# Optimization experiments

Measured on AMD Instinct MI355X. Metric: run time of the kernel, lower is better.

## Reference

```python
import jax, jax.numpy as jnp
import numpy as np

N, D, H = 8192, 64, 256

def setup_inputs() -> dict:
    key = jax.random.key(0)
    k0, k1, k2, k3, k4 = jax.random.split(key, 5)
    y = jax.random.normal(k0, (N, D), jnp.float32)
    t = jax.random.uniform(k1, (1,), jnp.float32)
    # diffeq MLP params (time-conditioned 1-hidden-layer tanh net)
    W1 = jax.random.normal(k2, (D, H), jnp.float32) / np.float32(np.sqrt(D))
    b1 = jnp.zeros((H,), jnp.float32)
    wt = jax.random.normal(k3, (H,), jnp.float32) * jnp.float32(0.1)
    W2 = jax.random.normal(k4, (H, D), jnp.float32) / np.float32(np.sqrt(H))
    b2 = jnp.zeros((D,), jnp.float32)
    return {"t": t, "y": y, "W1": W1, "b1": b1, "wt": wt, "W2": W2, "b2": b2}

def reference(t, y, W1, b1, wt, W2, b2):
    ts = t[0]

    def f_single(yi):  # yi: [D] -> dy_i: [D]
        h = jnp.tanh(yi @ W1 + ts * wt + b1)
        return h @ W2 + b2

    # dy = diffeq(t, y): batched forward pass
    h = jnp.tanh(y @ W1 + ts * wt + b1)          # [N, H]
    dy = h @ W2 + b2                              # [N, D]

    # brute-force divergence = trace of per-sample Jacobian d(dy_i)/d(y_i)
    # (replaces the O(D) looped torch.autograd.grad calls with one batched
    #  forward-mode Jacobian computation)
    div = jax.vmap(lambda yi: jnp.trace(jax.jacfwd(f_single)(yi)))(y)  # [N]

    # original returns (dy, -divergence.view(N,1)); concatenated for a single output
    return jnp.concatenate([dy, -div[:, None]], axis=1)  # [N, D+1]
```

## Files before the change

### kernel.cpp

```cpp
#include <hip/hip_runtime.h>

#define NROWS 8192
#define DDIM 64
#define HDIM 256
#define W1S 260
#define W2S 68
#define HPAD 264

using bf16x8 = __attribute__((ext_vector_type(8))) short;
using f32x4  = __attribute__((ext_vector_type(4))) float;

__device__ __forceinline__ unsigned short f2bf(float x) {
    unsigned u = __float_as_uint(x);
    u += 0x7FFFu + ((u >> 16) & 1u);
    return (unsigned short)(u >> 16);
}
__device__ __forceinline__ unsigned pack2(float a, float b) {
    return (unsigned)f2bf(a) | ((unsigned)f2bf(b) << 16);
}
__device__ __forceinline__ float fast_tanh(float x) {
    float e = __expf(2.0f * x);
    return 1.0f - 2.0f * __builtin_amdgcn_rcpf(e + 1.0f);
}

__global__ __launch_bounds__(256)
void ode_fused(const float* __restrict__ t,
               const float* __restrict__ y,
               const float* __restrict__ W1,
               const float* __restrict__ b1,
               const float* __restrict__ wt,
               const float* __restrict__ W2,
               const float* __restrict__ b2,
               float* __restrict__ out) {
    const int tid  = threadIdx.x;
    const int w    = tid >> 6;
    const int lane = tid & 63;
    const int l16  = lane & 15;
    const int quad = lane >> 4;
    const int row0 = blockIdx.x * 16;

    __shared__ __align__(16) unsigned short w1s[64 * W1S];
    __shared__ __align__(16) unsigned short w2s[256 * W2S];
    __shared__ __align__(16) unsigned short h_lds[16 * HPAD];
    __shared__ float svs[HDIM];
    __shared__ float dvp[64];

    const float4* W1v = (const float4*)W1;
    const float4* W2v = (const float4*)W2;
    #pragma unroll
    for (int i = 0; i < 16; ++i) {
        float4 f = W1v[i * 256 + tid];
        int p = (i * 256 + tid) * 4;
        unsigned* dst = (unsigned*)&w1s[(p >> 8) * W1S + (p & 255)];
        dst[0] = pack2(f.x, f.y); dst[1] = pack2(f.z, f.w);
    }
    #pragma unroll
    for (int i = 0; i < 16; ++i) {
        float4 f = W2v[i * 256 + tid];
        int p = (i * 256 + tid) * 4;
        unsigned* dst = (unsigned*)&w2s[(p >> 6) * W2S + (p & 63)];
        dst[0] = pack2(f.x, f.y); dst[1] = pack2(f.z, f.w);
    }
    {
        float s = 0.f;
        #pragma unroll
        for (int k = 0; k < DDIM; ++k) s += W1[k * HDIM + tid] * W2[tid * DDIM + k];
        svs[tid] = s;
    }

    bf16x8 afr[2];
    const float* yrow = y + (size_t)(row0 + l16) * DDIM;
    #pragma unroll
    for (int ks = 0; ks < 2; ++ks) {
        float4 f0 = *(const float4*)(yrow + ks * 32 + quad * 8);
        float4 f1 = *(const float4*)(yrow + ks * 32 + quad * 8 + 4);
        bf16x8 a;
        a[0]=(short)f2bf(f0.x); a[1]=(short)f2bf(f0.y); a[2]=(short)f2bf(f0.z); a[3]=(short)f2bf(f0.w);
        a[4]=(short)f2bf(f1.x); a[5]=(short)f2bf(f1.y); a[6]=(short)f2bf(f1.z); a[7]=(short)f2bf(f1.w);
        afr[ks] = a;
    }

    const float ts = t[0];
    float cbv[4];
    #pragma unroll
    for (int ct = 0; ct < 4; ++ct) {
        int m = w * 64 + ct * 16 + l16;
        cbv[ct] = b1[m] + ts * wt[m];
    }
    const int ncol = w * 16 + l16;
    const float b2v = b2[ncol];

    __syncthreads();

    f32x4 acc[4];
    #pragma unroll
    for (int ct = 0; ct < 4; ++ct) acc[ct] = (f32x4){0.f, 0.f, 0.f, 0.f};
    #pragma unroll
    for (int ct = 0; ct < 4; ++ct) {
        const int m = w * 64 + ct * 16 + l16;
        #pragma unroll
        for (int ks = 0; ks < 2; ++ks) {
            bf16x8 b;
            #pragma unroll
            for (int j = 0; j < 8; ++j)
                b[j] = (short)w1s[(ks * 32 + quad * 8 + j) * W1S + m];
            acc[ct] = __builtin_amdgcn_mfma_f32_16x16x32_bf16(afr[ks], b, acc[ct], 0, 0, 0);
        }
    }

    float dv[4] = {0.f, 0.f, 0.f, 0.f};
    #pragma unroll
    for (int ct = 0; ct < 4; ++ct) {
        const int m = w * 64 + ct * 16 + l16;
        const float sv = svs[m];
        #pragma unroll
        for (int r = 0; r < 4; ++r) {
            float z = acc[ct][r] + cbv[ct];
            float h = fast_tanh(z);
            dv[r] += (1.f - h * h) * sv;
            h_lds[(quad * 4 + r) * HPAD + m] = f2bf(h);
        }
    }
    #pragma unroll
    for (int off = 8; off; off >>= 1) {
        #pragma unroll
        for (int r = 0; r < 4; ++r) dv[r] += __shfl_down(dv[r], off, 16);
    }
    if (l16 == 0) {
        #pragma unroll
        for (int r = 0; r < 4; ++r) dvp[w * 16 + quad * 4 + r] = dv[r];
    }
    __syncthreads();

    f32x4 acc2 = (f32x4){0.f, 0.f, 0.f, 0.f};
    #pragma unroll
    for (int ks = 0; ks < 8; ++ks) {
        bf16x8 a = *(const bf16x8*)(&h_lds[l16 * HPAD + ks * 32 + quad * 8]);
        bf16x8 b;
        #pragma unroll
        for (int j = 0; j < 8; ++j)
            b[j] = (short)w2s[(ks * 32 + quad * 8 + j) * W2S + ncol];
        acc2 = __builtin_amdgcn_mfma_f32_16x16x32_bf16(a, b, acc2, 0, 0, 0);
    }
    #pragma unroll
    for (int r = 0; r < 4; ++r) {
        const int row = quad * 4 + r;
        out[(size_t)(row0 + row) * (DDIM + 1) + ncol] = acc2[r] + b2v;
    }

    if (w == 0 && lane < 16) {
        float s = dvp[lane] + dvp[16 + lane] + dvp[32 + lane] + dvp[48 + lane];
        out[(size_t)(row0 + lane) * (DDIM + 1) + DDIM] = -s;
    }
}

extern "C" void kernel_launch(void* const* d_in, const int* in_sizes, int n_in,
                              void* d_out, int out_size, void* d_ws, size_t ws_size,
                              hipStream_t stream) {
    const float* t  = (const float*)d_in[0];
    const float* y  = (const float*)d_in[1];
    const float* W1 = (const float*)d_in[2];
    const float* b1 = (const float*)d_in[3];
    const float* wt = (const float*)d_in[4];
    const float* W2 = (const float*)d_in[5];
    const float* b2 = (const float*)d_in[6];
    float* out = (float*)d_out;

    ode_fused<<<NROWS / 16, 256, 0, stream>>>(t, y, W1, b1, wt, W2, b2, out);
}
```

Measured before the change: 75.76 us.

## Load weight fragments directly from global into registers, drop LDS weight staging

Each thread now loads only the W1 and W2 elements its MFMA B-fragments need straight from global memory into registers, removing the full-weight bf16 staging in LDS. LDS usage falls to the hidden-activation tile and a few small buffers, which should allow more blocks per CU. The diagonal term W1^T·W2 is now computed with a 4-way split reduction using vector loads and shuffles. The cost is strided, uncoalesced global loads (stride HDIM or DDIM floats per element) that rely on L2 and cache hits, plus higher register pressure from holding 16 fragment vectors.

```diff
diff --git a/kernel.cpp b/kernel.cpp
--- a/kernel.cpp
+++ b/kernel.cpp
@@ -3,8 +3,6 @@
 #define NROWS 8192
 #define DDIM 64
 #define HDIM 256
-#define W1S 260
-#define W2S 68
 #define HPAD 264
 
 using bf16x8 = __attribute__((ext_vector_type(8))) short;
@@ -15,23 +13,20 @@
     u += 0x7FFFu + ((u >> 16) & 1u);
     return (unsigned short)(u >> 16);
 }
-__device__ __forceinline__ unsigned pack2(float a, float b) {
-    return (unsigned)f2bf(a) | ((unsigned)f2bf(b) << 16);
-}
 __device__ __forceinline__ float fast_tanh(float x) {
     float e = __expf(2.0f * x);
     return 1.0f - 2.0f * __builtin_amdgcn_rcpf(e + 1.0f);
 }
 
 __global__ __launch_bounds__(256)
-void ode_fused(const float* __restrict__ t,
-               const float* __restrict__ y,
-               const float* __restrict__ W1,
-               const float* __restrict__ b1,
-               const float* __restrict__ wt,
-               const float* __restrict__ W2,
-               const float* __restrict__ b2,
-               float* __restrict__ out) {
+void ode_slim(const float* __restrict__ t,
+              const float* __restrict__ y,
+              const float* __restrict__ W1,
+              const float* __restrict__ b1,
+              const float* __restrict__ wt,
+              const float* __restrict__ W2,
+              const float* __restrict__ b2,
+              float* __restrict__ out) {
     const int tid  = threadIdx.x;
     const int w    = tid >> 6;
     const int lane = tid & 63;
@@ -39,45 +34,70 @@
     const int quad = lane >> 4;
     const int row0 = blockIdx.x * 16;
 
-    __shared__ __align__(16) unsigned short w1s[64 * W1S];
-    __shared__ __align__(16) unsigned short w2s[256 * W2S];
     __shared__ __align__(16) unsigned short h_lds[16 * HPAD];
     __shared__ float svs[HDIM];
     __shared__ float dvp[64];
 
-    const float4* W1v = (const float4*)W1;
-    const float4* W2v = (const float4*)W2;
-    #pragma unroll
-    for (int i = 0; i < 16; ++i) {
-        float4 f = W1v[i * 256 + tid];
-        int p = (i * 256 + tid) * 4;
-        unsigned* dst = (unsigned*)&w1s[(p >> 8) * W1S + (p & 255)];
-        dst[0] = pack2(f.x, f.y); dst[1] = pack2(f.z, f.w);
-    }
-    #pragma unroll
-    for (int i = 0; i < 16; ++i) {
-        float4 f = W2v[i * 256 + tid];
-        int p = (i * 256 + tid) * 4;
-        unsigned* dst = (unsigned*)&w2s[(p >> 6) * W2S + (p & 63)];
-        dst[0] = pack2(f.x, f.y); dst[1] = pack2(f.z, f.w);
-    }
+    bf16x8 afr[2];
     {
-        float s = 0.f;
+        const float* yrow = y + (size_t)(row0 + l16) * DDIM;
         #pragma unroll
-        for (int k = 0; k < DDIM; ++k) s += W1[k * HDIM + tid] * W2[tid * DDIM + k];
-        svs[tid] = s;
+        for (int ks = 0; ks < 2; ++ks) {
+            float4 f0 = *(const float4*)(yrow + ks * 32 + quad * 8);
+            float4 f1 = *(const float4*)(yrow + ks * 32 + quad * 8 + 4);
+            bf16x8 a;
+            a[0]=(short)f2bf(f0.x); a[1]=(short)f2bf(f0.y); a[2]=(short)f2bf(f0.z); a[3]=(short)f2bf(f0.w);
+            a[4]=(short)f2bf(f1.x); a[5]=(short)f2bf(f1.y); a[6]=(short)f2bf(f1.z); a[7]=(short)f2bf(f1.w);
+            afr[ks] = a;
+        }
     }
 
-    bf16x8 afr[2];
-    const float* yrow = y + (size_t)(row0 + l16) * DDIM;
+    bf16x8 bfr1[4][2];
     #pragma unroll
-    for (int ks = 0; ks < 2; ++ks) {
-        float4 f0 = *(const float4*)(yrow + ks * 32 + quad * 8);
-        float4 f1 = *(const float4*)(yrow + ks * 32 + quad * 8 + 4);
-        bf16x8 a;
-        a[0]=(short)f2bf(f0.x); a[1]=(short)f2bf(f0.y); a[2]=(short)f2bf(f0.z); a[3]=(short)f2bf(f0.w);
-        a[4]=(short)f2bf(f1.x); a[5]=(short)f2bf(f1.y); a[6]=(short)f2bf(f1.z); a[7]=(short)f2bf(f1.w);
-        afr[ks] = a;
+    for (int ct = 0; ct < 4; ++ct) {
+        const int m = w * 64 + ct * 16 + l16;
+        #pragma unroll
+        for (int ks = 0; ks < 2; ++ks) {
+            const float* p = W1 + (size_t)(ks * 32 + quad * 8) * HDIM + m;
+            bf16x8 b;
+            #pragma unroll
+            for (int j = 0; j < 8; ++j) b[j] = (short)f2bf(p[j * HDIM]);
+            bfr1[ct][ks] = b;
+        }
+    }
+
+    const int ncol = w * 16 + l16;
+    bf16x8 bfr2[8];
+    #pragma unroll
+    for (int ks = 0; ks < 8; ++ks) {
+        const float* p = W2 + (size_t)(ks * 32 + quad * 8) * DDIM + ncol;
+        bf16x8 b;
+        #pragma unroll
+        for (int j = 0; j < 8; ++j) b[j] = (short)f2bf(p[j * DDIM]);
+        bfr2[ks] = b;
+    }
+
+    {
+        const int g   = tid >> 2;
+        const int sub = tid & 3;
+        #pragma unroll
+        for (int it = 0; it < 4; ++it) {
+            const int m = it * 64 + g;
+            float part = 0.f;
+            #pragma unroll
+            for (int s = 0; s < 4; ++s) {
+                const int k0 = s * 16 + sub * 4;
+                float4 w2v = *(const float4*)(W2 + m * DDIM + k0);
+                float a0 = W1[(k0 + 0) * HDIM + m];
+                float a1 = W1[(k0 + 1) * HDIM + m];
+                float a2 = W1[(k0 + 2) * HDIM + m];
+                float a3 = W1[(k0 + 3) * HDIM + m];
+                part += a0 * w2v.x + a1 * w2v.y + a2 * w2v.z + a3 * w2v.w;
+            }
+            part += __shfl_xor(part, 1);
+            part += __shfl_xor(part, 2);
+            if (sub == 0) svs[m] = part;
+        }
     }
 
     const float ts = t[0];
@@ -87,26 +107,18 @@
         int m = w * 64 + ct * 16 + l16;
         cbv[ct] = b1[m] + ts * wt[m];
     }
-    const int ncol = w * 16 + l16;
     const float b2v = b2[ncol];
-
-    __syncthreads();
 
     f32x4 acc[4];
     #pragma unroll
     for (int ct = 0; ct < 4; ++ct) acc[ct] = (f32x4){0.f, 0.f, 0.f, 0.f};
     #pragma unroll
-    for (int ct = 0; ct < 4; ++ct) {
-        const int m = w * 64 + ct * 16 + l16;
+    for (int ct = 0; ct < 4; ++ct)
         #pragma unroll
-        for (int ks = 0; ks < 2; ++ks) {
-            bf16x8 b;
-            #pragma unroll
-            for (int j = 0; j < 8; ++j)
-                b[j] = (short)w1s[(ks * 32 + quad * 8 + j) * W1S + m];
-            acc[ct] = __builtin_amdgcn_mfma_f32_16x16x32_bf16(afr[ks], b, acc[ct], 0, 0, 0);
-        }
-    }
+        for (int ks = 0; ks < 2; ++ks)
+            acc[ct] = __builtin_amdgcn_mfma_f32_16x16x32_bf16(afr[ks], bfr1[ct][ks], acc[ct], 0, 0, 0);
+
+    __syncthreads();
 
     float dv[4] = {0.f, 0.f, 0.f, 0.f};
     #pragma unroll
@@ -136,11 +148,7 @@
     #pragma unroll
     for (int ks = 0; ks < 8; ++ks) {
         bf16x8 a = *(const bf16x8*)(&h_lds[l16 * HPAD + ks * 32 + quad * 8]);
-        bf16x8 b;
-        #pragma unroll
-        for (int j = 0; j < 8; ++j)
-            b[j] = (short)w2s[(ks * 32 + quad * 8 + j) * W2S + ncol];
-        acc2 = __builtin_amdgcn_mfma_f32_16x16x32_bf16(a, b, acc2, 0, 0, 0);
+        acc2 = __builtin_amdgcn_mfma_f32_16x16x32_bf16(a, bfr2[ks], acc2, 0, 0, 0);
     }
     #pragma unroll
     for (int r = 0; r < 4; ++r) {
@@ -166,5 +174,5 @@
     const float* b2 = (const float*)d_in[6];
     float* out = (float*)d_out;
 
-    ode_fused<<<NROWS / 16, 256, 0, stream>>>(t, y, W1, b1, wt, W2, b2, out);
+    ode_slim<<<NROWS / 16, 256, 0, stream>>>(t, y, W1, b1, wt, W2, b2, out);
 }
```

Result: no change. 75.85 us (+0.1%).
